# Performance work log

Measured on AMD Instinct MI355X. Metric: run time of the kernel, lower is better.

The kernel has to match this reference:

```python
import math
import jax, jax.numpy as jnp
import numpy as np

N_HEADS = 16
NUM_BUCKETS = 32
MAX_DISTANCE = 128
ROTARY_BASE = 10000.0


def rotate_half(x):
    x1, x2 = jnp.split(x, 2, axis=-1)
    return jnp.concatenate((-x2, x1), axis=-1)


def rotary_freqs(T, dim):
    inv_freq = 1.0 / (ROTARY_BASE ** (jnp.arange(0, dim, 2, dtype=jnp.float32) / dim))
    t = jnp.arange(T, dtype=jnp.float32)
    freqs = jnp.einsum('i,j->ij', t, inv_freq)  # [T, dim/2]
    return jnp.concatenate((freqs, freqs), axis=-1)  # [T, dim]


def rel_pos_bucket_causal(rel_pos, num_buckets=NUM_BUCKETS, max_distance=MAX_DISTANCE):
    n = jnp.maximum(-rel_pos, 0)  # [T, T] int
    max_exact = num_buckets // 2
    is_small = n < max_exact
    n_safe = jnp.maximum(n, 1).astype(jnp.float32)
    val_if_large = max_exact + (
        jnp.log(n_safe / max_exact) / math.log(max_distance / max_exact) * (num_buckets - max_exact)
    ).astype(jnp.int32)
    val_if_large = jnp.minimum(val_if_large, num_buckets - 1)
    return jnp.where(is_small, n, val_if_large)


def setup_inputs() -> dict:
    key = jax.random.key(0)
    ks = jax.random.split(key, 10)
    B, T, C = 2, 2048, 1024
    s = 0.02
    return {
        'x':  jax.random.normal(ks[0], (B, T, C), dtype=jnp.float32),
        'Wq': jax.random.normal(ks[1], (C, C), dtype=jnp.float32) * s,
        'bq': jnp.zeros((C,), dtype=jnp.float32),
        'Wk': jax.random.normal(ks[2], (C, C), dtype=jnp.float32) * s,
        'bk': jnp.zeros((C,), dtype=jnp.float32),
        'Wv': jax.random.normal(ks[3], (C, C), dtype=jnp.float32) * s,
        'bv': jnp.zeros((C,), dtype=jnp.float32),
        'Wp': jax.random.normal(ks[4], (C, C), dtype=jnp.float32) * s,
        'bp': jnp.zeros((C,), dtype=jnp.float32),
        'rel_bias_table': jax.random.normal(ks[5], (NUM_BUCKETS, N_HEADS), dtype=jnp.float32) * s,
    }


def reference(x, Wq, bq, Wk, bk, Wv, bv, Wp, bp, rel_bias_table):
    B, T, C = x.shape
    H = N_HEADS
    D = C // H

    def heads(y):
        return y.reshape(B, T, H, D).transpose(0, 2, 1, 3)  # [B,H,T,D]

    q = heads(x @ Wq + bq)
    k = heads(x @ Wk + bk)
    v = heads(x @ Wv + bv)

    # rotary (use_xpos=False -> scale=1)
    freqs = rotary_freqs(T, D)  # [T, D]
    cos, sin = jnp.cos(freqs), jnp.sin(freqs)
    q = q * cos + rotate_half(q) * sin
    k = k * cos + rotate_half(k) * sin

    # relative position bias (causal, scale=1.0)
    pos = jnp.arange(T)
    rel_pos = pos[None, :] - pos[:, None]  # k_pos - q_pos
    bucket = rel_pos_bucket_causal(rel_pos)  # [T, T]
    bias = rel_bias_table[bucket]  # [T, T, H]
    bias = bias.transpose(2, 0, 1)  # [H, T, T]

    att = jnp.einsum('bhid,bhjd->bhij', q, k) + bias[None]
    att = att * (1.0 / math.sqrt(D))
    causal = pos[None, :] <= pos[:, None]  # tril mask [T, T]
    att = jnp.where(causal[None, None], att, -jnp.inf)
    att = jax.nn.softmax(att, axis=-1)

    y = jnp.einsum('bhij,bhjd->bhid', att, v)  # [B,H,T,D]
    y = y.transpose(0, 2, 1, 3).reshape(B, T, C)
    return y @ Wp + bp
```

## Files before the change

### kernel.cpp

```cpp
#include <hip/hip_runtime.h>
#include <hip/hip_bf16.h>
#include <math.h>

#define B_ 2
#define T_ 2048
#define C_ 1024
#define H_ 16
#define D_ 64
#define M_ (B_ * T_)
#define K_ 1024

#define SCALE2 0.18033688011112043f

typedef short bf16x8 __attribute__((ext_vector_type(8)));
typedef float f32x4  __attribute__((ext_vector_type(4)));
typedef unsigned int u32;

__device__ __forceinline__ unsigned short f2b(float f) {
    __hip_bfloat16 h = __float2bfloat16(f);
    return *reinterpret_cast<unsigned short*>(&h);
}
__device__ __forceinline__ u32 pack_bf16_rnd(float a, float b) {
    const u32 au = __float_as_uint(a) + 0x8000u;
    const u32 bu = __float_as_uint(b) + 0x8000u;
    return __builtin_amdgcn_perm(bu, au, 0x07060302u);
}
__device__ __forceinline__ void load_lds16(const void* g, void* l) {
    __builtin_amdgcn_global_load_lds(
        (const __attribute__((address_space(1))) u32*)g,
        (__attribute__((address_space(3))) u32*)l, 16, 0, 0);
}

__global__ __launch_bounds__(256) void prep(
    const float* __restrict__ x,
    const float* __restrict__ W0, const float* __restrict__ W1,
    const float* __restrict__ W2, const float* __restrict__ W3,
    const float* __restrict__ tbl,
    unsigned short* __restrict__ xb,
    unsigned short* __restrict__ T0, unsigned short* __restrict__ T1,
    unsigned short* __restrict__ T2, unsigned short* __restrict__ T3,
    float* __restrict__ dtab, float2* __restrict__ trig)
{
    __shared__ __align__(16) unsigned short tile[64][66];
    const int bx = blockIdx.x;
    const int tid = threadIdx.x;

    if (bx < 2048) {
        const int idx = bx * 256 + tid;
        const float4 a = reinterpret_cast<const float4*>(x)[idx * 2];
        const float4 b = reinterpret_cast<const float4*>(x)[idx * 2 + 1];
        unsigned short t[8] = {f2b(a.x), f2b(a.y), f2b(a.z), f2b(a.w),
                               f2b(b.x), f2b(b.y), f2b(b.z), f2b(b.w)};
        reinterpret_cast<bf16x8*>(xb)[idx] = *reinterpret_cast<const bf16x8*>(t);
    } else if (bx < 3072) {
        const int w = bx - 2048;
        const int z = w >> 8;
        const int rem = w & 255;
        const int k0 = (rem & 15) * 64, n0 = (rem >> 4) * 64;
        const float* W = z == 0 ? W0 : z == 1 ? W1 : z == 2 ? W2 : W3;
        unsigned short* Wt = z == 0 ? T0 : z == 1 ? T1 : z == 2 ? T2 : T3;

        #pragma unroll
        for (int it = 0; it < 4; ++it) {
            const int idx = it * 256 + tid;
            const int r = idx >> 4, c = (idx & 15) * 4;
            const float4 w4 = *reinterpret_cast<const float4*>(W + (size_t)(k0 + r) * C_ + n0 + c);
            tile[r][c + 0] = f2b(w4.x); tile[r][c + 1] = f2b(w4.y);
            tile[r][c + 2] = f2b(w4.z); tile[r][c + 3] = f2b(w4.w);
        }
        __syncthreads();
        #pragma unroll
        for (int it = 0; it < 2; ++it) {
            const int idx = it * 256 + tid;
            const int nc = idx >> 3, kc = (idx & 7) * 8;
            unsigned short tmp[8];
            #pragma unroll
            for (int e = 0; e < 8; ++e) tmp[e] = tile[kc + e][nc];
            *reinterpret_cast<bf16x8*>(Wt + (size_t)(n0 + nc) * K_ + k0 + kc) =
                *reinterpret_cast<const bf16x8*>(tmp);
        }
    } else {
        const int idx = (bx - 3072) * 256 + tid;
        if (idx < H_ * T_) {
            const int h = idx >> 11, n = idx & (T_ - 1);
            int bucket;
            if (n < 16) bucket = n;
            else {
                int vb = 16 + (int)(log2f((float)n * 0.0625f) * (16.0f / 3.0f));
                bucket = vb < 31 ? vb : 31;
            }
            dtab[idx] = tbl[bucket * H_ + h] * SCALE2;
        }
        const int t = idx >> 5, j = idx & 31;
        const float inv = exp2f(-(float)j * (13.287712379549449f / 32.0f));
        const float ang = (float)t * inv;
        trig[idx] = make_float2(cosf(ang), sinf(ang));
    }
}

template<int BN>
__device__ __forceinline__ void gemm_core(
    const unsigned short* __restrict__ A, const unsigned short* __restrict__ Bt,
    const float* __restrict__ bias, const float2* __restrict__ trig,
    float rot_scale, float* __restrict__ outf,
    unsigned short* __restrict__ outb, int mode, int m0, int n0)
{
    constexpr int FN  = BN / 32;
    constexpr int BCH = BN / 64;
    constexpr int NLD = 2 + BCH;
    __shared__ __align__(16) unsigned short As0[128 * 32];
    __shared__ __align__(16) unsigned short As1[128 * 32];
    __shared__ __align__(16) unsigned short As2[128 * 32];
    __shared__ __align__(16) unsigned short Bs0[BN * 32];
    __shared__ __align__(16) unsigned short Bs1[BN * 32];
    __shared__ __align__(16) unsigned short Bs2[BN * 32];

    const int tid = threadIdx.x;
    const int wid = tid >> 6, lane = tid & 63;
    const int l16 = lane & 15, quad = lane >> 4;
    const int wm = wid >> 1, wn = wid & 1;
    const int cs = ((quad ^ ((l16 >> 1) & 3)) * 8);

    f32x4 acc[4][FN];
    #pragma unroll
    for (int i = 0; i < 4; ++i)
        #pragma unroll
        for (int j = 0; j < FN; ++j) acc[i][j] = (f32x4){0.f, 0.f, 0.f, 0.f};

    auto stage = [&](unsigned short* Asb, unsigned short* Bsb, int k0) {
        #pragma unroll
        for (int it = 0; it < 2; ++it) {
            const int idx = it * 256 + tid;
            const int row = idx >> 2;
            const int ch = (((idx & 3) ^ ((idx >> 3) & 3)) * 8);
            load_lds16(A + (size_t)(m0 + row) * K_ + k0 + ch,
                       (char*)Asb + it * 4096 + wid * 1024);
        }
        #pragma unroll
        for (int it = 0; it < BCH; ++it) {
            const int idx = it * 256 + tid;
            const int row = idx >> 2;
            const int ch = (((idx & 3) ^ ((idx >> 3) & 3)) * 8);
            load_lds16(Bt + (size_t)(n0 + row) * K_ + k0 + ch,
                       (char*)Bsb + it * 4096 + wid * 1024);
        }
    };
    auto compute = [&](const unsigned short* Asb, const unsigned short* Bsb) {
        bf16x8 af[4], bf[FN];
        #pragma unroll
        for (int i = 0; i < 4; ++i)
            af[i] = *reinterpret_cast<const bf16x8*>(&Asb[(wm * 64 + i * 16 + l16) * 32 + cs]);
        #pragma unroll
        for (int j = 0; j < FN; ++j)
            bf[j] = *reinterpret_cast<const bf16x8*>(&Bsb[(wn * (BN / 2) + j * 16 + l16) * 32 + cs]);
        #pragma unroll
        for (int i = 0; i < 4; ++i)
            #pragma unroll
            for (int j = 0; j < FN; ++j)
                acc[i][j] = __builtin_amdgcn_mfma_f32_16x16x32_bf16(af[i], bf[j], acc[i][j], 0, 0, 0);
    };
    auto step = [&](const unsigned short* cA, const unsigned short* cB,
                    unsigned short* nA, unsigned short* nB, int kn, bool do_stage) {
        if constexpr (NLD == 4) asm volatile("s_waitcnt vmcnt(4)" ::: "memory");
        else                    asm volatile("s_waitcnt vmcnt(3)" ::: "memory");
        __builtin_amdgcn_s_barrier();
        __builtin_amdgcn_sched_barrier(0);
        if (do_stage) stage(nA, nB, kn);
        compute(cA, cB);
    };

    stage(As0, Bs0, 0);
    stage(As1, Bs1, 32);

    for (int kb = 0; kb < 30; kb += 3) {
        step(As0, Bs0, As2, Bs2, (kb + 2) * 32, true);
        step(As1, Bs1, As0, Bs0, (kb + 3) * 32, true);
        step(As2, Bs2, As1, Bs1, (kb + 4) * 32, true);
    }
    step(As0, Bs0, As2, Bs2, 0, false);
    asm volatile("s_waitcnt vmcnt(0)" ::: "memory");
    __builtin_amdgcn_s_barrier();
    __builtin_amdgcn_sched_barrier(0);
    compute(As1, Bs1);

    if (mode == 1) {
        #pragma unroll
        for (int i = 0; i < 4; ++i) {
            const int mb = m0 + wm * 64 + i * 16 + quad * 4;
            const int bb = mb >> 11, tb = mb & (T_ - 1);
            #pragma unroll
            for (int jc = 0; jc < FN / 2; ++jc) {
                const int n_lo = n0 + wn * (BN / 2) + jc * 16 + l16;
                const int h = n_lo >> 6, d = n_lo & 63;
                const float bv_lo = bias[n_lo], bv_hi = bias[n_lo + 32];
                unsigned short* po = outb + (((size_t)bb * H_ + h) * T_ + tb) * D_ + d;
                #pragma unroll
                for (int r = 0; r < 4; ++r) {
                    const float2 cs2 = trig[(tb + r) * 32 + d];
                    const float a = acc[i][jc][r] + bv_lo;
                    const float b = acc[i][jc + FN / 2][r] + bv_hi;
                    po[(size_t)r * D_]      = f2b((a * cs2.x - b * cs2.y) * rot_scale);
                    po[(size_t)r * D_ + 32] = f2b((b * cs2.x + a * cs2.y) * rot_scale);
                }
            }
        }
        return;
    }

    #pragma unroll
    for (int i = 0; i < 4; ++i) {
        const int mb = m0 + wm * 64 + i * 16 + quad * 4;
        #pragma unroll
        for (int j = 0; j < FN; ++j) {
            const int n = n0 + wn * (BN / 2) + j * 16 + l16;
            const float bv = bias[n];
            if (mode == 2) {
                const int bb = mb >> 11, t = mb & (T_ - 1);
                const int h = n >> 6, d = n & 63;
                uint2 w;
                w.x = pack_bf16_rnd(acc[i][j][0] + bv, acc[i][j][1] + bv);
                w.y = pack_bf16_rnd(acc[i][j][2] + bv, acc[i][j][3] + bv);
                *reinterpret_cast<uint2*>(
                    outb + (((size_t)bb * H_ + h) * D_ + d) * T_ + t) = w;
            } else {
                #pragma unroll
                for (int r = 0; r < 4; ++r)
                    outf[(size_t)(mb + r) * C_ + n] = acc[i][j][r] + bv;
            }
        }
    }
}

__global__ __launch_bounds__(256) void gemm_qkv(
    const unsigned short* __restrict__ A,
    const unsigned short* __restrict__ Wq, const unsigned short* __restrict__ Wk,
    const unsigned short* __restrict__ Wv,
    const float* __restrict__ bq, const float* __restrict__ bk,
    const float* __restrict__ bv, const float2* __restrict__ trig,
    unsigned short* __restrict__ Qo, unsigned short* __restrict__ Ko,
    unsigned short* __restrict__ Vto)
{
    const int lin = (int)blockIdx.x;
    const int g = lin & 7, slot = lin >> 3;
    const int w = g * 96 + slot;
    const int z = w >> 8, rem = w & 255;
    const int m0 = (rem >> 3) * 128, n0 = (rem & 7) * 128;

    const unsigned short* Bt = z == 0 ? Wq : z == 1 ? Wk : Wv;
    const float* bias = z == 0 ? bq : z == 1 ? bk : bv;
    unsigned short* outb = z == 0 ? Qo : z == 1 ? Ko : Vto;
    const float rs = z == 0 ? SCALE2 : 1.0f;
    gemm_core<128>(A, Bt, bias, trig, rs, nullptr, outb, z == 2 ? 2 : 1, m0, n0);
}

__global__ __launch_bounds__(256) void gemm_proj(
    const unsigned short* __restrict__ A, const unsigned short* __restrict__ Bt,
    const float* __restrict__ bias, float* __restrict__ outf)
{
    const int lin = (int)blockIdx.x;
    const int g = lin & 7, slot = lin >> 3;
    const int w = g * 64 + slot;
    const int m0 = (w >> 4) * 128, n0 = (w & 15) * 64;
    gemm_core<64>(A, Bt, bias, nullptr, 1.0f, outf, nullptr, 0, m0, n0);
}

__device__ __forceinline__ int kv_swz(int row, int col8) {
    return row * 64 + ((col8 ^ ((row ^ (row >> 2)) & 7)) * 8);
}

__global__ __launch_bounds__(256, 3) void flash_attn(
    const unsigned short* __restrict__ Q, const unsigned short* __restrict__ K,
    const unsigned short* __restrict__ Vt, const float* __restrict__ dtab,
    unsigned short* __restrict__ Y)
{
    __shared__ __align__(16) unsigned short Ks[2][64 * 64];
    __shared__ __align__(16) unsigned short Vs[2][64 * 64];
    __shared__ __align__(16) unsigned short Ps[4][16][72];
    __shared__ __align__(16) float bias_ls[64 + T_];

    const int lin = (int)blockIdx.x;
    const int bh  = lin & 31;
    const int qt  = 31 - (lin >> 5);
    const int h = bh & (H_ - 1), b = bh >> 4;
    const int tid = threadIdx.x;
    const int wid = tid >> 6, lane = tid & 63;
    const int l16 = lane & 15, quad = lane >> 4;
    const size_t base = (size_t)bh * T_ * D_;
    const size_t vbase = (size_t)bh * D_ * T_;
    const int q0 = qt * 64;

    if (tid < 64) bias_ls[tid] = -INFINITY;
    for (int ii = tid; ii < q0 + 64; ii += 256) bias_ls[64 + ii] = dtab[h * T_ + ii];

    bf16x8 ones;
    #pragma unroll
    for (int e = 0; e < 8; ++e) ones[e] = (short)0x3F80;

    const int sr0 = tid >> 3,         sc80 = tid & 7;
    const int sr1 = (tid + 256) >> 3, sc81 = (tid + 256) & 7;
    const int wo0 = kv_swz(sr0, sc80), wo1 = kv_swz(sr1, sc81);
    const int sch0 = sc80 * 8, sch1 = sc81 * 8;

    int kro[4][2], vro[4][2];
    #pragma unroll
    for (int c = 0; c < 4; ++c)
        #pragma unroll
        for (int s = 0; s < 2; ++s) {
            kro[c][s] = kv_swz(l16 * 4 + c, s * 4 + quad);
            vro[c][s] = kv_swz(c * 16 + l16, s * 4 + quad);
        }

    bf16x8 kr[2], vr[2];
    kr[0] = *reinterpret_cast<const bf16x8*>(K + base + (size_t)sr0 * D_ + sch0);
    kr[1] = *reinterpret_cast<const bf16x8*>(K + base + (size_t)sr1 * D_ + sch1);
    vr[0] = *reinterpret_cast<const bf16x8*>(Vt + vbase + (size_t)sr0 * T_ + sch0);
    vr[1] = *reinterpret_cast<const bf16x8*>(Vt + vbase + (size_t)sr1 * T_ + sch1);
    *reinterpret_cast<bf16x8*>(&Ks[0][wo0]) = kr[0];
    *reinterpret_cast<bf16x8*>(&Ks[0][wo1]) = kr[1];
    *reinterpret_cast<bf16x8*>(&Vs[0][wo0]) = vr[0];
    *reinterpret_cast<bf16x8*>(&Vs[0][wo1]) = vr[1];
    kr[0] = *reinterpret_cast<const bf16x8*>(K + base + (size_t)(64 + sr0) * D_ + sch0);
    kr[1] = *reinterpret_cast<const bf16x8*>(K + base + (size_t)(64 + sr1) * D_ + sch1);
    vr[0] = *reinterpret_cast<const bf16x8*>(Vt + vbase + (size_t)sr0 * T_ + 64 + sch0);
    vr[1] = *reinterpret_cast<const bf16x8*>(Vt + vbase + (size_t)sr1 * T_ + 64 + sch1);
    __syncthreads();

    const int arow = q0 + wid * 16 + l16;
    const int crow = q0 + wid * 16 + quad * 4;
    const int nbase = crow - l16 * 4;

    bf16x8 qf[2];
    qf[0] = *reinterpret_cast<const bf16x8*>(Q + base + (size_t)arow * D_ + quad * 8);
    qf[1] = *reinterpret_cast<const bf16x8*>(Q + base + (size_t)arow * D_ + 32 + quad * 8);

    f32x4 o[4], ol;
    #pragma unroll
    for (int c = 0; c < 4; ++c) o[c] = (f32x4){0.f, 0.f, 0.f, 0.f};
    ol = (f32x4){0.f, 0.f, 0.f, 0.f};

    for (int kt = 0; kt <= qt; ++kt) {
        const int j0 = kt * 64;
        const int cur = kt & 1, nxt = cur ^ 1;

        if (kt < qt) {
            *reinterpret_cast<bf16x8*>(&Ks[nxt][wo0]) = kr[0];
            *reinterpret_cast<bf16x8*>(&Ks[nxt][wo1]) = kr[1];
            *reinterpret_cast<bf16x8*>(&Vs[nxt][wo0]) = vr[0];
            *reinterpret_cast<bf16x8*>(&Vs[nxt][wo1]) = vr[1];
        }
        if (kt < qt - 1) {
            const int jn = j0 + 128;
            kr[0] = *reinterpret_cast<const bf16x8*>(K + base + (size_t)(jn + sr0) * D_ + sch0);
            kr[1] = *reinterpret_cast<const bf16x8*>(K + base + (size_t)(jn + sr1) * D_ + sch1);
            vr[0] = *reinterpret_cast<const bf16x8*>(Vt + vbase + (size_t)sr0 * T_ + jn + sch0);
            vr[1] = *reinterpret_cast<const bf16x8*>(Vt + vbase + (size_t)sr1 * T_ + jn + sch1);
        }

        const int d0 = nbase - j0;
        const f32x4 blo = *reinterpret_cast<const f32x4*>(&bias_ls[60 + d0]);
        const f32x4 bhi = *reinterpret_cast<const f32x4*>(&bias_ls[64 + d0]);

        f32x4 sc[4];
        #pragma unroll
        for (int c = 0; c < 4; ++c) {
            #pragma unroll
            for (int r = 0; r < 4; ++r)
                sc[c][r] = (r >= c) ? bhi[r - c] : blo[4 + r - c];
        }
        __builtin_amdgcn_s_setprio(1);
        #pragma unroll
        for (int c = 0; c < 4; ++c) {
            #pragma unroll
            for (int s = 0; s < 2; ++s) {
                bf16x8 kf = *reinterpret_cast<const bf16x8*>(&Ks[cur][kro[c][s]]);
                sc[c] = __builtin_amdgcn_mfma_f32_16x16x32_bf16(qf[s], kf, sc[c], 0, 0, 0);
            }
        }
        __builtin_amdgcn_s_setprio(0);

        #pragma unroll
        for (int r = 0; r < 4; ++r) {
            const float p0 = __builtin_amdgcn_exp2f(sc[0][r]);
            const float p1 = __builtin_amdgcn_exp2f(sc[1][r]);
            const float p2 = __builtin_amdgcn_exp2f(sc[2][r]);
            const float p3 = __builtin_amdgcn_exp2f(sc[3][r]);
            uint2 w;
            w.x = pack_bf16_rnd(p0, p1);
            w.y = pack_bf16_rnd(p2, p3);
            *reinterpret_cast<uint2*>(&Ps[wid][quad * 4 + r][l16 * 4]) = w;
        }

        __builtin_amdgcn_s_setprio(1);
        #pragma unroll
        for (int s = 0; s < 2; ++s) {
            bf16x8 pf = *reinterpret_cast<const bf16x8*>(&Ps[wid][l16][s * 32 + quad * 8]);
            #pragma unroll
            for (int c = 0; c < 4; ++c) {
                bf16x8 vf = *reinterpret_cast<const bf16x8*>(&Vs[cur][vro[c][s]]);
                o[c] = __builtin_amdgcn_mfma_f32_16x16x32_bf16(pf, vf, o[c], 0, 0, 0);
            }
            ol = __builtin_amdgcn_mfma_f32_16x16x32_bf16(pf, ones, ol, 0, 0, 0);
        }
        __builtin_amdgcn_s_setprio(0);

        if (kt < qt) {
            asm volatile("s_waitcnt lgkmcnt(0)" ::: "memory");
            __builtin_amdgcn_s_barrier();
            __builtin_amdgcn_sched_barrier(0);
        }
    }

    #pragma unroll
    for (int r = 0; r < 4; ++r) {
        const int i = crow + r;
        const float invl = 1.0f / ol[r];
        #pragma unroll
        for (int c = 0; c < 4; ++c)
            Y[((size_t)b * T_ + i) * C_ + h * D_ + c * 16 + l16] = f2b(o[c][r] * invl);
    }
}

extern "C" void kernel_launch(void* const* d_in, const int* in_sizes, int n_in,
                              void* d_out, int out_size, void* d_ws, size_t ws_size,
                              hipStream_t stream)
{
    const float* x   = (const float*)d_in[0];
    const float* Wq  = (const float*)d_in[1];
    const float* bq  = (const float*)d_in[2];
    const float* Wk  = (const float*)d_in[3];
    const float* bk  = (const float*)d_in[4];
    const float* Wv  = (const float*)d_in[5];
    const float* bv  = (const float*)d_in[6];
    const float* Wp  = (const float*)d_in[7];
    const float* bp  = (const float*)d_in[8];
    const float* tbl = (const float*)d_in[9];
    float* out = (float*)d_out;

    const size_t n1 = (size_t)B_ * H_ * T_ * D_;
    const size_t nW = (size_t)C_ * C_;
    unsigned short* xb  = (unsigned short*)d_ws;
    unsigned short* Wqt = xb + (size_t)M_ * K_;
    unsigned short* Wkt = Wqt + nW;
    unsigned short* Wvt = Wkt + nW;
    unsigned short* Wpt = Wvt + nW;
    unsigned short* Qb  = Wpt + nW;
    unsigned short* Kb  = Qb + n1;
    unsigned short* Vtb = Kb + n1;
    unsigned short* Yb  = Vtb + n1;
    float* dtab = (float*)(Yb + n1);
    float2* trig = (float2*)(dtab + H_ * T_);

    const dim3 blk(256);

    prep<<<dim3(3328), blk, 0, stream>>>(x, Wq, Wk, Wv, Wp, tbl,
                                         xb, Wqt, Wkt, Wvt, Wpt, dtab, trig);

    gemm_qkv<<<dim3(768), blk, 0, stream>>>(
        xb, Wqt, Wkt, Wvt, bq, bk, bv, trig, Qb, Kb, Vtb);

    flash_attn<<<dim3(1024), blk, 0, stream>>>(Qb, Kb, Vtb, dtab, Yb);

    gemm_proj<<<dim3(512), blk, 0, stream>>>(Yb, Wpt, bp, out);
}
```

Baseline: 186.5 us.

## Drop LDS bias staging, prefetch bias from global, swizzle P buffer, raise occupancy

The relative-position bias table is now laid out in global memory with a -inf pad per head. The attention kernel prefetches the next tile's bias values into registers from global memory instead of first copying the whole per-head bias row into LDS. The P staging buffer is shrunk to 64-wide rows with an XOR swizzle in place of row padding, which cuts LDS use enough to raise launch bounds from 3 to 4 blocks per SIMD. The intent is to remove the per-block bias preload and its LDS footprint and gain occupancy, at the cost of per-iteration global loads and possible register pressure under the tighter bound.

Measured after the change: 191.0 us. 2.4% more time.

```diff
diff --git a/kernel.cpp b/kernel.cpp
--- a/kernel.cpp
+++ b/kernel.cpp
@@ -81,18 +81,22 @@
         }
     } else {
         const int idx = (bx - 3072) * 256 + tid;
-        if (idx < H_ * T_) {
-            const int h = idx >> 11, n = idx & (T_ - 1);
-            int bucket;
-            if (n < 16) bucket = n;
-            else {
-                int vb = 16 + (int)(log2f((float)n * 0.0625f) * (16.0f / 3.0f));
-                bucket = vb < 31 ? vb : 31;
+        {
+            const int h = idx >> 12, j = idx & 4095;
+            if (j < 64) dtab[idx] = -INFINITY;
+            else if (j < 64 + T_) {
+                const int n = j - 64;
+                int bucket;
+                if (n < 16) bucket = n;
+                else {
+                    int vb = 16 + (int)(log2f((float)n * 0.0625f) * (16.0f / 3.0f));
+                    bucket = vb < 31 ? vb : 31;
+                }
+                dtab[idx] = tbl[bucket * H_ + h] * SCALE2;
             }
-            dtab[idx] = tbl[bucket * H_ + h] * SCALE2;
-        }
-        const int t = idx >> 5, j = idx & 31;
-        const float inv = exp2f(-(float)j * (13.287712379549449f / 32.0f));
+        }
+        const int t = idx >> 5, j2 = idx & 31;
+        const float inv = exp2f(-(float)j2 * (13.287712379549449f / 32.0f));
         const float ang = (float)t * inv;
         trig[idx] = make_float2(cosf(ang), sinf(ang));
     }
@@ -268,15 +272,14 @@
     return row * 64 + ((col8 ^ ((row ^ (row >> 2)) & 7)) * 8);
 }
 
-__global__ __launch_bounds__(256, 3) void flash_attn(
+__global__ __launch_bounds__(256, 4) void flash_attn(
     const unsigned short* __restrict__ Q, const unsigned short* __restrict__ K,
     const unsigned short* __restrict__ Vt, const float* __restrict__ dtab,
     unsigned short* __restrict__ Y)
 {
     __shared__ __align__(16) unsigned short Ks[2][64 * 64];
     __shared__ __align__(16) unsigned short Vs[2][64 * 64];
-    __shared__ __align__(16) unsigned short Ps[4][16][72];
-    __shared__ __align__(16) float bias_ls[64 + T_];
+    __shared__ __align__(16) unsigned short Ps[4][1024];
 
     const int lin = (int)blockIdx.x;
     const int bh  = lin & 31;
@@ -289,9 +292,6 @@
     const size_t vbase = (size_t)bh * D_ * T_;
     const int q0 = qt * 64;
 
-    if (tid < 64) bias_ls[tid] = -INFINITY;
-    for (int ii = tid; ii < q0 + 64; ii += 256) bias_ls[64 + ii] = dtab[h * T_ + ii];
-
     bf16x8 ones;
     #pragma unroll
     for (int e = 0; e < 8; ++e) ones[e] = (short)0x3F80;
@@ -309,6 +309,23 @@
             kro[c][s] = kv_swz(l16 * 4 + c, s * 4 + quad);
             vro[c][s] = kv_swz(c * 16 + l16, s * 4 + quad);
         }
+
+    unsigned short* PsW = Ps[wid];
+    int pwo[4], pro[2];
+    #pragma unroll
+    for (int r = 0; r < 4; ++r) {
+        const int row = quad * 4 + r;
+        pwo[r] = row * 64 + (((l16 >> 1) ^ (row & 7)) << 3) + ((l16 & 1) << 2);
+    }
+    #pragma unroll
+    for (int s = 0; s < 2; ++s)
+        pro[s] = l16 * 64 + (((s * 4 + quad) ^ (l16 & 7)) << 3);
+
+    const int arow = q0 + wid * 16 + l16;
+    const int crow = q0 + wid * 16 + quad * 4;
+    const int nbase = crow - l16 * 4;
+
+    const float* bg = dtab + (h << 12) + 64 + nbase;
 
     bf16x8 kr[2], vr[2];
     kr[0] = *reinterpret_cast<const bf16x8*>(K + base + (size_t)sr0 * D_ + sch0);
@@ -323,11 +340,9 @@
     kr[1] = *reinterpret_cast<const bf16x8*>(K + base + (size_t)(64 + sr1) * D_ + sch1);
     vr[0] = *reinterpret_cast<const bf16x8*>(Vt + vbase + (size_t)sr0 * T_ + 64 + sch0);
     vr[1] = *reinterpret_cast<const bf16x8*>(Vt + vbase + (size_t)sr1 * T_ + 64 + sch1);
+    f32x4 bplo = *reinterpret_cast<const f32x4*>(bg - 4);
+    f32x4 bphi = *reinterpret_cast<const f32x4*>(bg);
     __syncthreads();
-
-    const int arow = q0 + wid * 16 + l16;
-    const int crow = q0 + wid * 16 + quad * 4;
-    const int nbase = crow - l16 * 4;
 
     bf16x8 qf[2];
     qf[0] = *reinterpret_cast<const bf16x8*>(Q + base + (size_t)arow * D_ + quad * 8);
@@ -341,6 +356,8 @@
     for (int kt = 0; kt <= qt; ++kt) {
         const int j0 = kt * 64;
         const int cur = kt & 1, nxt = cur ^ 1;
+
+        const f32x4 blo = bplo, bhi = bphi;
 
         if (kt < qt) {
             *reinterpret_cast<bf16x8*>(&Ks[nxt][wo0]) = kr[0];
@@ -355,10 +372,11 @@
             vr[0] = *reinterpret_cast<const bf16x8*>(Vt + vbase + (size_t)sr0 * T_ + jn + sch0);
             vr[1] = *reinterpret_cast<const bf16x8*>(Vt + vbase + (size_t)sr1 * T_ + jn + sch1);
         }
-
-        const int d0 = nbase - j0;
-        const f32x4 blo = *reinterpret_cast<const f32x4*>(&bias_ls[60 + d0]);
-        const f32x4 bhi = *reinterpret_cast<const f32x4*>(&bias_ls[64 + d0]);
+        if (kt < qt) {
+            const float* bn = bg - (j0 + 64);
+            bplo = *reinterpret_cast<const f32x4*>(bn - 4);
+            bphi = *reinterpret_cast<const f32x4*>(bn);
+        }
 
         f32x4 sc[4];
         #pragma unroll
@@ -387,13 +405,13 @@
             uint2 w;
             w.x = pack_bf16_rnd(p0, p1);
             w.y = pack_bf16_rnd(p2, p3);
-            *reinterpret_cast<uint2*>(&Ps[wid][quad * 4 + r][l16 * 4]) = w;
+            *reinterpret_cast<uint2*>(PsW + pwo[r]) = w;
         }
 
         __builtin_amdgcn_s_setprio(1);
         #pragma unroll
         for (int s = 0; s < 2; ++s) {
-            bf16x8 pf = *reinterpret_cast<const bf16x8*>(&Ps[wid][l16][s * 32 + quad * 8]);
+            bf16x8 pf = *reinterpret_cast<const bf16x8*>(PsW + pro[s]);
             #pragma unroll
             for (int c = 0; c < 4; ++c) {
                 bf16x8 vf = *reinterpret_cast<const bf16x8*>(&Vs[cur][vro[c][s]]);
@@ -448,7 +466,7 @@
     unsigned short* Vtb = Kb + n1;
     unsigned short* Yb  = Vtb + n1;
     float* dtab = (float*)(Yb + n1);
-    float2* trig = (float2*)(dtab + H_ * T_);
+    float2* trig = (float2*)(dtab + (size_t)H_ * 4096);
 
     const dim3 blk(256);
 
```
